# Optimization experiments

Hardware: AMD Instinct MI355X
Metric: run time of the kernel (lower is better)

## Reference

```python
import jax, jax.numpy as jnp
import numpy as np

EPS = 1e-6


def setup_inputs() -> dict:
    key = jax.random.key(0)
    kx, kw = jax.random.split(key)
    B, C, N = 8, 256, 2048
    x = jax.random.normal(kx, (B, C, N), dtype=jnp.float32)
    # nn.Linear(dim*2, 2, bias=False): weight shape [2, 2*C]
    W = jax.random.normal(kw, (2, 2 * C), dtype=jnp.float32) * (1.0 / np.sqrt(2 * C))
    return {"x": x, "W": W}


def reference(x, W):
    B, C, N = x.shape
    # cosine similarity matrix [B, N, N]
    sim = jnp.einsum('bcn,bcm->bnm', x, x)
    # torch: sqrt(sum(x^2 + 1e-6, dim=1)) -> eps added per-channel before sum
    norms = jnp.sqrt(jnp.sum(x * x + EPS, axis=1))            # [B, N]
    io_abs = sim / (norms[:, :, None] * norms[:, None, :])    # [B, N, N]
    # zero the diagonal (fill_diagonal_(0)) before argmax
    io_abs = io_abs * (1.0 - jnp.eye(N, dtype=io_abs.dtype))
    idx = jnp.argmax(io_abs, axis=2)                          # [B, N] nearest-neighbor per token
    # gather retrieved features: f_re[b, :, n] = x[b, :, idx[b, n]]
    f_re = jnp.take_along_axis(x, idx[:, None, :], axis=2)    # [B, C, N]
    # gated fusion
    fus = jnp.concatenate([x, f_re], axis=1).transpose(0, 2, 1)  # [B, N, 2C]
    w = jax.nn.softmax(fus @ W.T, axis=-1)                    # [B, N, 2]
    w = w.transpose(0, 2, 1)                                  # [B, 2, N]
    out = x * w[:, 0:1, :] + f_re * w[:, 1:2, :]
    return (out, f_re)
```

## Files before the change

kernel.cpp:

```cpp
#include <hip/hip_runtime.h>
#include <hip/hip_bf16.h>
#include <math.h>

constexpr int B_ = 8;
constexpr int C_ = 256;
constexpr int N_ = 2048;
constexpr int CN_ = C_ * N_;
constexpr int TOT_ = B_ * C_ * N_;
constexpr int NTILES = 16;
constexpr int NPAIRS = 136;

typedef __attribute__((ext_vector_type(8))) short bf16x8;
typedef __attribute__((ext_vector_type(4))) float f32x4;

__device__ __forceinline__ void g2l16(const void* g, void* l) {
    __builtin_amdgcn_global_load_lds(
        (const __attribute__((address_space(1))) void*)g,
        (__attribute__((address_space(3))) void*)l, 16, 0, 0);
}

__device__ __forceinline__ unsigned short bits(__hip_bfloat16 h) {
    union { __hip_bfloat16 b; unsigned short u; } cv;
    cv.b = h;
    return cv.u;
}

__device__ __forceinline__ float b2f(short s) {
    union { float f; unsigned u; } cv;
    cv.u = ((unsigned)(unsigned short)s) << 16;
    return cv.f;
}

__device__ __forceinline__ unsigned long long packkey(float v, int m) {
    const unsigned b = __float_as_uint(v);
    const unsigned u = (b & 0x80000000u) ? ~b : (b | 0x80000000u);
    return ((unsigned long long)u << 32) | (unsigned)(2047 - m);
}

__global__ __launch_bounds__(256) void convert_kernel(const float* __restrict__ x,
                                                      __hip_bfloat16* __restrict__ hiT,
                                                      __hip_bfloat16* __restrict__ loT,
                                                      float* __restrict__ normacc) {
    const int blk = blockIdx.x;
    const int batch = blk & 7;
    const int nt = (blk >> 3) & 31;
    const int ctile = blk >> 8;
    const int n0 = nt << 6, c0 = ctile << 6;
    const int t = threadIdx.x;
    const int i = t & 63, j = t >> 6;

    __shared__ float tb[64][65];
    __shared__ float red[4][64];

    float s = 0.f;
    const float* xp = x + (size_t)batch * CN_ + (size_t)c0 * N_ + n0 + i;
#pragma unroll 4
    for (int r = 0; r < 16; ++r) {
        const int cl = j + r * 4;
        const float v = xp[(size_t)cl * N_];
        tb[cl][i] = v;
        s += v * v;
    }
    red[j][i] = s;
    __syncthreads();

    const int cp = t & 31;
    const int c2 = cp << 1;
    const int nb = t >> 5;
#pragma unroll 4
    for (int r = 0; r < 8; ++r) {
        const int n = nb + r * 8;
        const float v0 = tb[c2][n], v1 = tb[c2 + 1][n];
        const size_t o = ((size_t)batch * N_ + n0 + n) * C_ + c0 + c2;
        const __hip_bfloat16 h0 = __float2bfloat16(v0);
        const __hip_bfloat16 h1 = __float2bfloat16(v1);
        const __hip_bfloat16 g0 = __float2bfloat16(v0 - __bfloat162float(h0));
        const __hip_bfloat16 g1 = __float2bfloat16(v1 - __bfloat162float(h1));
        ((unsigned*)hiT)[o >> 1] = ((unsigned)bits(h1) << 16) | bits(h0);
        ((unsigned*)loT)[o >> 1] = ((unsigned)bits(g1) << 16) | bits(g0);
    }
    if (j == 0) {
        const float tt = red[0][i] + red[1][i] + red[2][i] + red[3][i];
        atomicAdd(normacc + batch * N_ + n0 + i, tt);
    }
}

__global__ void rnorm_fin_kernel(const float* __restrict__ normacc,
                                 float* __restrict__ rnorm) {
    const int t = blockIdx.x * 256 + threadIdx.x;
    rnorm[t] = 1.0f / sqrtf(normacc[t] + 256.0f * 1e-6f);
}

__global__ __launch_bounds__(256, 2) void gram_mfma_kernel(
        const __hip_bfloat16* __restrict__ hiT, const __hip_bfloat16* __restrict__ loT,
        const float* __restrict__ rnorm,
        float* __restrict__ pval, int* __restrict__ pidx, float* __restrict__ pval2) {
    const int blk = blockIdx.x;
    const int batch = blk & 7;
    int p = blk >> 3;
    int bn = 0;
    while (p >= NTILES - bn) { p -= NTILES - bn; ++bn; }
    const int bm = bn + p;
    const bool diag = (bn == bm);
    const int n0 = bn << 7, m0 = bm << 7;

    __shared__ short As0[128 * 64];
    __shared__ short As1[128 * 64];
    __shared__ short Bs0[128 * 64];
    __shared__ short Bs1[128 * 64];
    short* ov = &As0[0];
    float (*rv1)[2] = (float(*)[2])(ov + 0);
    int (*ri1)[2] = (int(*)[2])(ov + 512);
    float (*rv2)[2] = (float(*)[2])(ov + 1024);
    float (*cv1)[2] = (float(*)[2])(ov + 1536);
    int (*ci1)[2] = (int(*)[2])(ov + 2048);
    float (*cv2)[2] = (float(*)[2])(ov + 2560);
    float* rnA = (float*)(ov + 3072);

    const int tid = threadIdx.x;
    const int l = tid & 63, w = tid >> 6;
    const int lm = l & 15, q = l >> 4;
    const int x7 = lm & 7;
    const int wn = (w >> 1) << 6, wm = (w & 1) << 6;

    const size_t bbase = (size_t)batch * CN_;
    const short* gA[4];
    const short* gB[4];
    int ldsoff[4];
#pragma unroll
    for (int pp = 0; pp < 4; ++pp) {
        const int slot = tid + pp * 256;
        const int r = slot >> 3, sidx = slot & 7;
        const int sw = sidx ^ (r & 7);
        const short* base = (const short*)((sw < 4) ? hiT : loT);
        gA[pp] = base + bbase + (size_t)(n0 + r) * C_ + (sw & 3) * 8;
        gB[pp] = base + bbase + (size_t)(m0 + r) * C_ + (sw & 3) * 8;
        ldsoff[pp] = slot * 8;
    }
    int aoff[8], boff[8];
#pragma unroll
    for (int rt = 0; rt < 4; ++rt) {
        const int ra = wn + rt * 16 + lm;
        const int rb = wm + rt * 16 + lm;
        aoff[rt * 2] = ra * 64 + ((q ^ x7) * 8);
        aoff[rt * 2 + 1] = ra * 64 + (((4 | q) ^ x7) * 8);
        boff[rt * 2] = rb * 64 + ((q ^ x7) * 8);
        boff[rt * 2 + 1] = rb * 64 + (((4 | q) ^ x7) * 8);
    }

    f32x4 acc[4][4];
#pragma unroll
    for (int rt = 0; rt < 4; ++rt)
#pragma unroll
        for (int ct = 0; ct < 4; ++ct) acc[rt][ct] = (f32x4){0.f, 0.f, 0.f, 0.f};

#pragma unroll
    for (int pp = 0; pp < 4; ++pp) {
        g2l16(gA[pp], As0 + ldsoff[pp]);
        g2l16(gB[pp], Bs0 + ldsoff[pp]);
    }
    __syncthreads();

#pragma unroll
    for (int kt = 0; kt < 8; ++kt) {
        short* Ac = (kt & 1) ? As1 : As0;
        short* Bc = (kt & 1) ? Bs1 : Bs0;
        if (kt < 7) {
            short* An = (kt & 1) ? As0 : As1;
            short* Bn = (kt & 1) ? Bs0 : Bs1;
#pragma unroll
            for (int pp = 0; pp < 4; ++pp) {
                g2l16(gA[pp] + (kt + 1) * 32, An + ldsoff[pp]);
                g2l16(gB[pp] + (kt + 1) * 32, Bn + ldsoff[pp]);
            }
        }
        bf16x8 ah[4], al[4], bh[4], bl[4];
#pragma unroll
        for (int rt = 0; rt < 4; ++rt) {
            ah[rt] = *(const bf16x8*)(Ac + aoff[rt * 2]);
            al[rt] = *(const bf16x8*)(Ac + aoff[rt * 2 + 1]);
        }
#pragma unroll
        for (int ct = 0; ct < 4; ++ct) {
            bh[ct] = *(const bf16x8*)(Bc + boff[ct * 2]);
            bl[ct] = *(const bf16x8*)(Bc + boff[ct * 2 + 1]);
        }
#pragma unroll
        for (int rt = 0; rt < 4; ++rt)
#pragma unroll
            for (int ct = 0; ct < 4; ++ct) {
                acc[rt][ct] = __builtin_amdgcn_mfma_f32_16x16x32_bf16(
                    ah[rt], bh[ct], acc[rt][ct], 0, 0, 0);
                acc[rt][ct] = __builtin_amdgcn_mfma_f32_16x16x32_bf16(
                    ah[rt], bl[ct], acc[rt][ct], 0, 0, 0);
                acc[rt][ct] = __builtin_amdgcn_mfma_f32_16x16x32_bf16(
                    al[rt], bh[ct], acc[rt][ct], 0, 0, 0);
            }
        __syncthreads();
    }

    if (tid < 128) rnA[tid] = rnorm[batch * N_ + n0 + tid];

    float rnm[4];
#pragma unroll
    for (int ct = 0; ct < 4; ++ct) rnm[ct] = rnorm[batch * N_ + m0 + wm + ct * 16 + lm];

#pragma unroll
    for (int rt = 0; rt < 4; ++rt) {
#pragma unroll
        for (int r = 0; r < 4; ++r) {
            const int nrow = n0 + wn + rt * 16 + q * 4 + r;
            float v1 = -3.4e38f, v2 = -3.4e38f;
            int i1 = 0x7fffffff;
#pragma unroll
            for (int ct = 0; ct < 4; ++ct) {
                const int m = m0 + wm + ct * 16 + lm;
                const float v = acc[rt][ct][r] * rnm[ct];
                if (m == nrow) continue;
                if (v > v1) { v2 = v1; v1 = v; i1 = m; }
                else if (v > v2) v2 = v;
            }
#pragma unroll
            for (int d = 1; d < 16; d <<= 1) {
                const float ov1 = __shfl_xor(v1, d, 64);
                const int oi1 = __shfl_xor(i1, d, 64);
                const float ov2 = __shfl_xor(v2, d, 64);
                if (ov1 > v1 || (ov1 == v1 && oi1 < i1)) {
                    v2 = fmaxf(v1, ov2); v1 = ov1; i1 = oi1;
                } else {
                    v2 = fmaxf(v2, ov1);
                }
            }
            if (lm == 0) {
                const int rloc = wn + rt * 16 + q * 4 + r;
                rv1[rloc][w & 1] = v1;
                ri1[rloc][w & 1] = i1;
                rv2[rloc][w & 1] = v2;
            }
        }
    }
    __syncthreads();

    if (!diag) {
        float rnn[4][4];
#pragma unroll
        for (int rt = 0; rt < 4; ++rt)
#pragma unroll
            for (int r = 0; r < 4; ++r) rnn[rt][r] = rnA[wn + rt * 16 + q * 4 + r];
#pragma unroll
        for (int ct = 0; ct < 4; ++ct) {
            float v1 = -3.4e38f, v2 = -3.4e38f;
            int i1 = 0x7fffffff;
#pragma unroll
            for (int rt = 0; rt < 4; ++rt) {
#pragma unroll
                for (int r = 0; r < 4; ++r) {
                    const float v = acc[rt][ct][r] * rnn[rt][r];
                    const int nn = n0 + wn + rt * 16 + q * 4 + r;
                    if (v > v1) { v2 = v1; v1 = v; i1 = nn; }
                    else if (v > v2) v2 = v;
                }
            }
#pragma unroll
            for (int d = 16; d < 64; d <<= 1) {
                const float ov1 = __shfl_xor(v1, d, 64);
                const int oi1 = __shfl_xor(i1, d, 64);
                const float ov2 = __shfl_xor(v2, d, 64);
                if (ov1 > v1 || (ov1 == v1 && oi1 < i1)) {
                    v2 = fmaxf(v1, ov2); v1 = ov1; i1 = oi1;
                } else {
                    v2 = fmaxf(v2, ov1);
                }
            }
            if (q == 0) {
                const int mloc = wm + ct * 16 + lm;
                cv1[mloc][w >> 1] = v1;
                ci1[mloc][w >> 1] = i1;
                cv2[mloc][w >> 1] = v2;
            }
        }
    }
    __syncthreads();

    if (tid < 128) {
        {
            float v1 = rv1[tid][0]; int i1 = ri1[tid][0]; float v2 = rv2[tid][0];
            const float ov1 = rv1[tid][1]; const int oi1 = ri1[tid][1]; const float ov2 = rv2[tid][1];
            if (ov1 > v1 || (ov1 == v1 && oi1 < i1)) { v2 = fmaxf(v1, ov2); v1 = ov1; i1 = oi1; }
            else v2 = fmaxf(v2, ov1);
            const size_t gi = (size_t)(batch * NTILES + bm) * N_ + n0 + tid;
            pval[gi] = v1; pidx[gi] = i1; pval2[gi] = v2;
        }
        if (!diag) {
            float v1 = cv1[tid][0]; int i1 = ci1[tid][0]; float v2 = cv2[tid][0];
            const float ov1 = cv1[tid][1]; const int oi1 = ci1[tid][1]; const float ov2 = cv2[tid][1];
            if (ov1 > v1 || (ov1 == v1 && oi1 < i1)) { v2 = fmaxf(v1, ov2); v1 = ov1; i1 = oi1; }
            else v2 = fmaxf(v2, ov1);
            const size_t gi = (size_t)(batch * NTILES + bn) * N_ + m0 + tid;
            pval[gi] = v1; pidx[gi] = i1; pval2[gi] = v2;
        }
    }
}

__global__ void combine_kernel(const float* __restrict__ pval, const int* __restrict__ pidx,
                               const float* __restrict__ pval2, int* __restrict__ fidx,
                               int* __restrict__ rcnt, int* __restrict__ ridx,
                               unsigned long long* __restrict__ pbest) {
    const int t = blockIdx.x * 256 + threadIdx.x;
    const int batch = t >> 11, n = t & 2047;
    float v1 = -3.4e38f, v2 = -3.4e38f;
    int i1 = 0x7fffffff;
    for (int s = 0; s < NTILES; ++s) {
        const size_t gi = (size_t)(batch * NTILES + s) * N_ + n;
        const float ov1 = pval[gi]; const int oi1 = pidx[gi]; const float ov2 = pval2[gi];
        if (ov1 > v1 || (ov1 == v1 && oi1 < i1)) { v2 = fmaxf(v1, ov2); v1 = ov1; i1 = oi1; }
        else v2 = fmaxf(v2, ov1);
    }
    fidx[t] = i1;
    if (v1 - v2 < 1e-4f) {
        const int slot = atomicAdd(rcnt, 1);
        ridx[slot] = t;
        pbest[slot] = 0ull;
    }
}

__global__ __launch_bounds__(256) void rescue_kernel(const float* __restrict__ x,
                                                     const float* __restrict__ rnorm,
                                                     const int* __restrict__ rcnt,
                                                     const int* __restrict__ ridx,
                                                     unsigned long long* __restrict__ pbest) {
    const int cnt = *rcnt;
    const int nwork = cnt << 3;
    const int tid = threadIdx.x;
    __shared__ unsigned long long bk[256];
    for (int wi = blockIdx.x; wi < nwork; wi += gridDim.x) {
        const int rr = wi >> 3, ch = wi & 7;
        const int t = ridx[rr];
        const int batch = t >> 11, n = t & 2047;
        const int m = (ch << 8) + tid;
        const float* xb = x + (size_t)batch * CN_;
        float s0 = 0.f, s1 = 0.f, s2 = 0.f, s3 = 0.f;
        const float* xn = xb + n;
        const float* xm = xb + m;
#pragma unroll 4
        for (int c = 0; c < C_; c += 4) {
            s0 += xn[(size_t)(c + 0) * N_] * xm[(size_t)(c + 0) * N_];
            s1 += xn[(size_t)(c + 1) * N_] * xm[(size_t)(c + 1) * N_];
            s2 += xn[(size_t)(c + 2) * N_] * xm[(size_t)(c + 2) * N_];
            s3 += xn[(size_t)(c + 3) * N_] * xm[(size_t)(c + 3) * N_];
        }
        const float v = ((s0 + s1) + (s2 + s3)) * rnorm[batch * N_ + m];
        bk[tid] = (m == n) ? 0ull : packkey(v, m);
        __syncthreads();
        for (int sft = 128; sft > 0; sft >>= 1) {
            if (tid < sft) {
                const unsigned long long o = bk[tid + sft];
                if (o > bk[tid]) bk[tid] = o;
            }
            __syncthreads();
        }
        if (tid == 0) atomicMax(&pbest[rr], bk[0]);
        __syncthreads();
    }
}

__global__ void rescue_fin_kernel(const unsigned long long* __restrict__ pbest,
                                  const int* __restrict__ rcnt,
                                  const int* __restrict__ ridx,
                                  int* __restrict__ fidx) {
    const int rr = blockIdx.x * 256 + threadIdx.x;
    if (rr < *rcnt) {
        const unsigned long long k = pbest[rr];
        const int m = 2047 - (int)(unsigned)(k & 0xffffffffull);
        fidx[ridx[rr]] = m;
    }
}

__global__ __launch_bounds__(256) void finish_kernel(const float* __restrict__ x,
                                                     const __hip_bfloat16* __restrict__ hiT,
                                                     const __hip_bfloat16* __restrict__ loT,
                                                     const float* __restrict__ W,
                                                     const int* __restrict__ fidx,
                                                     float* __restrict__ out) {
    const int batch = blockIdx.x & 7;
    const int nt = blockIdx.x >> 3;
    const int n0 = nt << 4;
    const int t = threadIdx.x;
    const int i = t & 15, cg = t >> 4;

    __shared__ float Wl[1024];
    __shared__ int il[16];
    __shared__ float l0r[16][17], l1r[16][17];
    __shared__ float w0s[16], w1s[16];

    for (int u = t; u < 1024; u += 256) Wl[u] = W[u];
    if (t < 16) il[t] = fidx[batch * N_ + n0 + t];
    __syncthreads();

    const float* xb = x + (size_t)batch * CN_ + n0 + i;
    const int myidx = il[i];
    const size_t row = ((size_t)batch * N_ + myidx) * C_ + cg * 16;

    float fvv[16];
    {
        const bf16x8* hp = (const bf16x8*)(hiT + row);
        const bf16x8* lp = (const bf16x8*)(loT + row);
#pragma unroll
        for (int v8 = 0; v8 < 2; ++v8) {
            const bf16x8 h = hp[v8];
            const bf16x8 g = lp[v8];
#pragma unroll
            for (int e = 0; e < 8; ++e) fvv[v8 * 8 + e] = b2f(h[e]) + b2f(g[e]);
        }
    }

    float l0 = 0.f, l1 = 0.f;
#pragma unroll
    for (int cc = 0; cc < 16; ++cc) {
        const int c = cg * 16 + cc;
        const float xv = xb[(size_t)c * N_];
        l0 += xv * Wl[c] + fvv[cc] * Wl[256 + c];
        l1 += xv * Wl[512 + c] + fvv[cc] * Wl[768 + c];
    }
    l0r[cg][i] = l0;
    l1r[cg][i] = l1;
    __syncthreads();
    if (t < 16) {
        float L0 = 0.f, L1 = 0.f;
#pragma unroll
        for (int g = 0; g < 16; ++g) { L0 += l0r[g][t]; L1 += l1r[g][t]; }
        const float mx = fmaxf(L0, L1);
        const float e0 = expf(L0 - mx);
        const float e1 = expf(L1 - mx);
        const float inv = 1.0f / (e0 + e1);
        w0s[t] = e0 * inv;
        w1s[t] = e1 * inv;
    }
    __syncthreads();
    const float w0 = w0s[i], w1 = w1s[i];

#pragma unroll
    for (int cc = 0; cc < 16; ++cc) {
        const int c = cg * 16 + cc;
        const size_t off = (size_t)batch * CN_ + (size_t)c * N_ + n0 + i;
        const float xv = xb[(size_t)c * N_];
        out[off] = xv * w0 + fvv[cc] * w1;
        out[TOT_ + off] = fvv[cc];
    }
}

extern "C" void kernel_launch(void* const* d_in, const int* in_sizes, int n_in,
                              void* d_out, int out_size, void* d_ws, size_t ws_size,
                              hipStream_t stream) {
    const float* x = (const float*)d_in[0];
    const float* W = (const float*)d_in[1];
    float* out = (float*)d_out;

    const size_t BF_BYTES = (size_t)TOT_ * 2;
    const size_t NORM_BYTES = (size_t)B_ * N_ * 4;
    const size_t P_BYTES = (size_t)B_ * NTILES * N_ * 4;

    uint8_t* p = (uint8_t*)d_ws;
    __hip_bfloat16* hiT = (__hip_bfloat16*)p; p += BF_BYTES;
    __hip_bfloat16* loT = (__hip_bfloat16*)p; p += BF_BYTES;
    float* rnorm = (float*)p; p += NORM_BYTES;
    float* normacc = (float*)p; p += NORM_BYTES;
    float* pval = (float*)p; p += P_BYTES;
    int* pidx = (int*)p; p += P_BYTES;
    float* pval2 = (float*)p; p += P_BYTES;
    int* fidx = (int*)p; p += NORM_BYTES;
    int* rcnt = (int*)p; p += 256;
    int* ridx = (int*)p; p += NORM_BYTES;
    unsigned long long* pbest = (unsigned long long*)p; p += (size_t)B_ * N_ * 8;

    hipMemsetAsync(rcnt, 0, 4, stream);
    hipMemsetAsync(normacc, 0, NORM_BYTES, stream);
    convert_kernel<<<1024, 256, 0, stream>>>(x, hiT, loT, normacc);
    rnorm_fin_kernel<<<64, 256, 0, stream>>>(normacc, rnorm);
    gram_mfma_kernel<<<B_ * NPAIRS, 256, 0, stream>>>(hiT, loT, rnorm, pval, pidx, pval2);
    combine_kernel<<<64, 256, 0, stream>>>(pval, pidx, pval2, fidx, rcnt, ridx, pbest);
    rescue_kernel<<<256, 256, 0, stream>>>(x, rnorm, rcnt, ridx, pbest);
    rescue_fin_kernel<<<64, 256, 0, stream>>>(pbest, rcnt, ridx, fidx);
    finish_kernel<<<1024, 256, 0, stream>>>(x, hiT, loT, W, fidx, out);
}
```

Measured before the change: 180.3 us.

## Deepen LDS prefetch pipeline with explicit waitcnt and barriers in sim GEMM

Restructures the K-loop of the similarity GEMM so that two K-tiles are in flight. After the fragments are read into registers and a barrier is passed, the next-next tile is loaded into the buffer just consumed, and fine-grained vmcnt waits replace the full __syncthreads. This is meant to hide global-to-LDS load latency behind the MFMA work. In exchange it relies on hand-placed s_waitcnt counts, which can break correctness if the count assumptions are wrong.

Result: no change. 178.7 us (-0.9%).

```diff
diff --git a/kernel.cpp b/kernel.cpp
--- a/kernel.cpp
+++ b/kernel.cpp
@@ -159,21 +159,20 @@
         g2l16(gA[pp], As0 + ldsoff[pp]);
         g2l16(gB[pp], Bs0 + ldsoff[pp]);
     }
-    __syncthreads();
+#pragma unroll
+    for (int pp = 0; pp < 4; ++pp) {
+        g2l16(gA[pp] + 32, As1 + ldsoff[pp]);
+        g2l16(gB[pp] + 32, Bs1 + ldsoff[pp]);
+    }
+    asm volatile("s_waitcnt vmcnt(8)" ::: "memory");
+    __builtin_amdgcn_sched_barrier(0);
+    __builtin_amdgcn_s_barrier();
+    __builtin_amdgcn_sched_barrier(0);
 
 #pragma unroll
     for (int kt = 0; kt < 8; ++kt) {
         short* Ac = (kt & 1) ? As1 : As0;
         short* Bc = (kt & 1) ? Bs1 : Bs0;
-        if (kt < 7) {
-            short* An = (kt & 1) ? As0 : As1;
-            short* Bn = (kt & 1) ? Bs0 : Bs1;
-#pragma unroll
-            for (int pp = 0; pp < 4; ++pp) {
-                g2l16(gA[pp] + (kt + 1) * 32, An + ldsoff[pp]);
-                g2l16(gB[pp] + (kt + 1) * 32, Bn + ldsoff[pp]);
-            }
-        }
         bf16x8 ah[4], al[4], bh[4], bl[4];
 #pragma unroll
         for (int rt = 0; rt < 4; ++rt) {
@@ -184,6 +183,17 @@
         for (int ct = 0; ct < 4; ++ct) {
             bh[ct] = *(const bf16x8*)(Bc + boff[ct * 2]);
             bl[ct] = *(const bf16x8*)(Bc + boff[ct * 2 + 1]);
+        }
+        asm volatile("s_waitcnt lgkmcnt(0)" ::: "memory");
+        __builtin_amdgcn_sched_barrier(0);
+        __builtin_amdgcn_s_barrier();
+        __builtin_amdgcn_sched_barrier(0);
+        if (kt < 6) {
+#pragma unroll
+            for (int pp = 0; pp < 4; ++pp) {
+                g2l16(gA[pp] + (kt + 2) * 32, Ac + ldsoff[pp]);
+                g2l16(gB[pp] + (kt + 2) * 32, Bc + ldsoff[pp]);
+            }
         }
 #pragma unroll
         for (int rt = 0; rt < 4; ++rt)
@@ -196,7 +206,16 @@
                 acc[rt][ct] = __builtin_amdgcn_mfma_f32_16x16x32_bf16(
                     al[rt], bh[ct], acc[rt][ct], 0, 0, 0);
             }
-        __syncthreads();
+        if (kt < 6) {
+            asm volatile("s_waitcnt vmcnt(8)" ::: "memory");
+        } else if (kt == 6) {
+            asm volatile("s_waitcnt vmcnt(0)" ::: "memory");
+        }
+        if (kt < 7) {
+            __builtin_amdgcn_sched_barrier(0);
+            __builtin_amdgcn_s_barrier();
+            __builtin_amdgcn_sched_barrier(0);
+        }
     }
 
     if (tid < 128) rnA[tid] = rnorm[batch * N_ + n0 + tid];
```

## Load Gram MFMA operands directly from global into registers, dropping LDS staging

Applied to the files above, without the earlier changes.

Removes the LDS double-buffered staging (global_load_lds into swizzled tiles plus __syncthreads) from the Gram matrix MFMA loop. Each lane now reads its bf16 hi/lo fragments straight from global memory into a two-deep register buffer, prefetching the next K step. This drops the barriers and LDS traffic and shrinks shared memory, which may allow more resident blocks. In exchange, every wave redundantly fetches operands from global/L2 (each A row is read by two waves, each B row by two), and register pressure rises.

Result: slower. 214.7 us (+19.1%).

```diff
diff --git a/kernel.cpp b/kernel.cpp
--- a/kernel.cpp
+++ b/kernel.cpp
@@ -12,12 +12,6 @@
 
 typedef __attribute__((ext_vector_type(8))) short bf16x8;
 typedef __attribute__((ext_vector_type(4))) float f32x4;
-
-__device__ __forceinline__ void g2l16(const void* g, void* l) {
-    __builtin_amdgcn_global_load_lds(
-        (const __attribute__((address_space(1))) void*)g,
-        (__attribute__((address_space(3))) void*)l, 16, 0, 0);
-}
 
 __device__ __forceinline__ unsigned short bits(__hip_bfloat16 h) {
     union { __hip_bfloat16 b; unsigned short u; } cv;
@@ -104,11 +98,8 @@
     const bool diag = (bn == bm);
     const int n0 = bn << 7, m0 = bm << 7;
 
-    __shared__ short As0[128 * 64];
-    __shared__ short As1[128 * 64];
-    __shared__ short Bs0[128 * 64];
-    __shared__ short Bs1[128 * 64];
-    short* ov = &As0[0];
+    __shared__ short epi[3328];
+    short* ov = &epi[0];
     float (*rv1)[2] = (float(*)[2])(ov + 0);
     int (*ri1)[2] = (int(*)[2])(ov + 512);
     float (*rv2)[2] = (float(*)[2])(ov + 1024);
@@ -120,32 +111,16 @@
     const int tid = threadIdx.x;
     const int l = tid & 63, w = tid >> 6;
     const int lm = l & 15, q = l >> 4;
-    const int x7 = lm & 7;
     const int wn = (w >> 1) << 6, wm = (w & 1) << 6;
 
     const size_t bbase = (size_t)batch * CN_;
-    const short* gA[4];
-    const short* gB[4];
-    int ldsoff[4];
-#pragma unroll
-    for (int pp = 0; pp < 4; ++pp) {
-        const int slot = tid + pp * 256;
-        const int r = slot >> 3, sidx = slot & 7;
-        const int sw = sidx ^ (r & 7);
-        const short* base = (const short*)((sw < 4) ? hiT : loT);
-        gA[pp] = base + bbase + (size_t)(n0 + r) * C_ + (sw & 3) * 8;
-        gB[pp] = base + bbase + (size_t)(m0 + r) * C_ + (sw & 3) * 8;
-        ldsoff[pp] = slot * 8;
-    }
-    int aoff[8], boff[8];
+    const char* hA = (const char*)(hiT + bbase);
+    const char* lA = (const char*)(loT + bbase);
+    int va[4], vb[4];
 #pragma unroll
     for (int rt = 0; rt < 4; ++rt) {
-        const int ra = wn + rt * 16 + lm;
-        const int rb = wm + rt * 16 + lm;
-        aoff[rt * 2] = ra * 64 + ((q ^ x7) * 8);
-        aoff[rt * 2 + 1] = ra * 64 + (((4 | q) ^ x7) * 8);
-        boff[rt * 2] = rb * 64 + ((q ^ x7) * 8);
-        boff[rt * 2 + 1] = rb * 64 + (((4 | q) ^ x7) * 8);
+        va[rt] = ((n0 + wn + rt * 16 + lm) << 9) + (q << 4);
+        vb[rt] = ((m0 + wm + rt * 16 + lm) << 9) + (q << 4);
     }
 
     f32x4 acc[4][4];
@@ -154,50 +129,36 @@
 #pragma unroll
         for (int ct = 0; ct < 4; ++ct) acc[rt][ct] = (f32x4){0.f, 0.f, 0.f, 0.f};
 
-#pragma unroll
-    for (int pp = 0; pp < 4; ++pp) {
-        g2l16(gA[pp], As0 + ldsoff[pp]);
-        g2l16(gB[pp], Bs0 + ldsoff[pp]);
-    }
-    __syncthreads();
-
+    bf16x8 Ah[2][4], Al[2][4], Bh[2][4], Bl[2][4];
+
+#define LOADK(BUF, KT)                                                    \
+    do {                                                                  \
+        _Pragma("unroll") for (int rt = 0; rt < 4; ++rt) {                \
+            Ah[BUF][rt] = *(const bf16x8*)(hA + va[rt] + (KT) * 64);      \
+            Al[BUF][rt] = *(const bf16x8*)(lA + va[rt] + (KT) * 64);      \
+            Bh[BUF][rt] = *(const bf16x8*)(hA + vb[rt] + (KT) * 64);      \
+            Bl[BUF][rt] = *(const bf16x8*)(lA + vb[rt] + (KT) * 64);      \
+        }                                                                 \
+    } while (0)
+
+    LOADK(0, 0);
 #pragma unroll
     for (int kt = 0; kt < 8; ++kt) {
-        short* Ac = (kt & 1) ? As1 : As0;
-        short* Bc = (kt & 1) ? Bs1 : Bs0;
-        if (kt < 7) {
-            short* An = (kt & 1) ? As0 : As1;
-            short* Bn = (kt & 1) ? Bs0 : Bs1;
-#pragma unroll
-            for (int pp = 0; pp < 4; ++pp) {
-                g2l16(gA[pp] + (kt + 1) * 32, An + ldsoff[pp]);
-                g2l16(gB[pp] + (kt + 1) * 32, Bn + ldsoff[pp]);
-            }
-        }
-        bf16x8 ah[4], al[4], bh[4], bl[4];
-#pragma unroll
-        for (int rt = 0; rt < 4; ++rt) {
-            ah[rt] = *(const bf16x8*)(Ac + aoff[rt * 2]);
-            al[rt] = *(const bf16x8*)(Ac + aoff[rt * 2 + 1]);
-        }
-#pragma unroll
-        for (int ct = 0; ct < 4; ++ct) {
-            bh[ct] = *(const bf16x8*)(Bc + boff[ct * 2]);
-            bl[ct] = *(const bf16x8*)(Bc + boff[ct * 2 + 1]);
-        }
+        const int b = kt & 1;
+        if (kt < 7) LOADK(b ^ 1, kt + 1);
 #pragma unroll
         for (int rt = 0; rt < 4; ++rt)
 #pragma unroll
             for (int ct = 0; ct < 4; ++ct) {
                 acc[rt][ct] = __builtin_amdgcn_mfma_f32_16x16x32_bf16(
-                    ah[rt], bh[ct], acc[rt][ct], 0, 0, 0);
+                    Ah[b][rt], Bh[b][ct], acc[rt][ct], 0, 0, 0);
                 acc[rt][ct] = __builtin_amdgcn_mfma_f32_16x16x32_bf16(
-                    ah[rt], bl[ct], acc[rt][ct], 0, 0, 0);
+                    Ah[b][rt], Bl[b][ct], acc[rt][ct], 0, 0, 0);
                 acc[rt][ct] = __builtin_amdgcn_mfma_f32_16x16x32_bf16(
-                    al[rt], bh[ct], acc[rt][ct], 0, 0, 0);
-            }
-        __syncthreads();
-    }
+                    Al[b][rt], Bh[b][ct], acc[rt][ct], 0, 0, 0);
+            }
+    }
+#undef LOADK
 
     if (tid < 128) rnA[tid] = rnorm[batch * N_ + n0 + tid];
 
```
